# Kernel tuning notes

Measured on AMD Instinct MI355X. Metric: run time of the kernel, lower is better.

The kernel has to match this reference:

```python
import jax, jax.numpy as jnp
import numpy as np

L, H, NH, NKV, HD, S, P, FF = 2, 2048, 16, 2, 128, 1024, 1024, 5632
G = NH // NKV
THETA = 1000000.0
EPS = 1e-6
SCALE = 1.0 / np.sqrt(HD).astype(np.float32)


def rms_norm(x, w):
    return x * jax.lax.rsqrt(jnp.mean(x * x, axis=-1, keepdims=True) + EPS) * w


def rotate_half(x):
    x1, x2 = jnp.split(x, 2, axis=-1)
    return jnp.concatenate([-x2, x1], axis=-1)


def setup_inputs() -> dict:
    key = jax.random.key(0)
    ks = iter(jax.random.split(key, 16))
    w = lambda shape: jax.random.normal(next(ks), shape, jnp.float32) * 0.02
    return {
        'inputs_embeds': jax.random.normal(next(ks), (1, S, H), jnp.float32),
        'position_ids': (jnp.arange(S, dtype=jnp.int32) + P)[None, :],
        'past_k': jax.random.normal(next(ks), (L, 1, NKV, P, HD), jnp.float32),
        'past_v': jax.random.normal(next(ks), (L, 1, NKV, P, HD), jnp.float32),
        'ln1_w': jnp.ones((L, H), jnp.float32),
        'wq': w((L, H, NH * HD)), 'bq': jnp.zeros((L, NH * HD), jnp.float32),
        'wk': w((L, H, NKV * HD)), 'bk': jnp.zeros((L, NKV * HD), jnp.float32),
        'wv': w((L, H, NKV * HD)), 'bv': jnp.zeros((L, NKV * HD), jnp.float32),
        'wo': w((L, NH * HD, H)),
        'ln2_w': jnp.ones((L, H), jnp.float32),
        'w_gate': w((L, H, FF)), 'w_up': w((L, H, FF)), 'w_down': w((L, FF, H)),
        'norm_w': jnp.ones((H,), jnp.float32),
    }


def reference(inputs_embeds, position_ids, past_k, past_v, ln1_w, wq, bq, wk, bk,
              wv, bv, wo, ln2_w, w_gate, w_up, w_down, norm_w):
    pos = position_ids.astype(jnp.float32)                      # [1,S]
    inv_freq = 1.0 / (THETA ** (jnp.arange(0, HD, 2, dtype=jnp.float32) / HD))
    freqs = pos[:, :, None] * inv_freq                          # [1,S,HD/2]
    emb = jnp.concatenate([freqs, freqs], axis=-1)              # [1,S,HD]
    cos = jnp.cos(emb)[:, None]                                 # [1,1,S,HD]
    sin = jnp.sin(emb)[:, None]
    T = P + S
    k_pos = jnp.arange(T, dtype=jnp.float32)
    # causal mask over absolute positions: future keys masked with -65504
    mask = jnp.where(k_pos[None, None, None, :] > pos[:, None, :, None],
                     jnp.float32(-65504.0), jnp.float32(0.0))   # [1,1,S,T]

    hidden = inputs_embeds
    present = []
    for i in range(L):
        residual = hidden
        h = rms_norm(hidden, ln1_w[i])
        q = (h @ wq[i] + bq[i]).reshape(1, S, NH, HD).transpose(0, 2, 1, 3)
        k = (h @ wk[i] + bk[i]).reshape(1, S, NKV, HD).transpose(0, 2, 1, 3)
        v = (h @ wv[i] + bv[i]).reshape(1, S, NKV, HD).transpose(0, 2, 1, 3)
        q = q * cos + rotate_half(q) * sin
        k = k * cos + rotate_half(k) * sin
        k = jnp.concatenate([past_k[i], k], axis=2)             # [1,NKV,T,HD]
        v = jnp.concatenate([past_v[i], v], axis=2)
        present.append(k)
        present.append(v)
        # GQA: group query heads per kv head instead of expanding k/v
        qg = q.reshape(1, NKV, G, S, HD)
        attn = jnp.einsum('bkgsd,bktd->bkgst', qg, k) * SCALE   # [1,NKV,G,S,T]
        attn = jax.nn.softmax(attn + mask[:, :, None], axis=-1)
        out = jnp.einsum('bkgst,bktd->bkgsd', attn, v)
        out = out.reshape(1, NH, S, HD).transpose(0, 2, 1, 3).reshape(1, S, H)
        hidden = residual + out @ wo[i]
        residual = hidden
        h = rms_norm(hidden, ln2_w[i])
        h = (jax.nn.silu(h @ w_gate[i]) * (h @ w_up[i])) @ w_down[i]
        hidden = residual + h
    hidden = rms_norm(hidden, norm_w)
    return (hidden, *present)
```

## Files before the change

kernel.cpp:

```cpp
#include <hip/hip_runtime.h>

#define L_ 2
#define H_ 2048
#define NH_ 16
#define NKV_ 2
#define HD_ 128
#define S_ 1024
#define P_ 1024
#define T_ 2048
#define FF_ 5632
#define QKVN_ 2560
#define KOFF_ 2048
#define VOFF_ 2304

#define EPS_ 1e-6f
#define SCALE_ 0.08838834764831845f
#define DEFER_THR_ 8.0f

typedef __bf16 bf16_t;
typedef unsigned int u32;
typedef __bf16 bx8 __attribute__((ext_vector_type(8)));
typedef __bf16 bx4 __attribute__((ext_vector_type(4)));
typedef float  fx4 __attribute__((ext_vector_type(4)));

__device__ __forceinline__ fx4 mfma16(bx8 a, bx8 b, fx4 c) {
  return __builtin_amdgcn_mfma_f32_16x16x32_bf16(a, b, c, 0, 0, 0);
}

#define GLL16(gsrc, ldst) __builtin_amdgcn_global_load_lds( \
    (__attribute__((address_space(1))) void*)(gsrc),        \
    (__attribute__((address_space(3))) void*)(ldst), 16, 0, 0)

__device__ __forceinline__ bx8 lds_read_b128(char* p) {
  u32 a = (u32)(uintptr_t)(__attribute__((address_space(3))) void*)p;
  bx8 d;
  asm volatile("ds_read_b128 %0, %1" : "=v"(d) : "v"(a));
  return d;
}
__device__ __forceinline__ void lds_write_b16(char* p, float v) {
  u32 a = (u32)(uintptr_t)(__attribute__((address_space(3))) void*)p;
  bf16_t b = (bf16_t)v;
  u32 d = (u32)__builtin_bit_cast(unsigned short, b);
  asm volatile("ds_write_b16 %0, %1" :: "v"(a), "v"(d));
}

__device__ __forceinline__ int xcd_swizzle(int orig, int nwg) {
  int q = nwg >> 3, r = nwg & 7;
  int xcd = orig & 7, lid = orig >> 3;
  return (xcd < r ? xcd * (q + 1) : r * (q + 1) + (xcd - r) * q) + lid;
}

__global__ void k_rope_tables(const int* __restrict__ pos, float* __restrict__ ct, float* __restrict__ st) {
  int i = blockIdx.x * 256 + threadIdx.x;
  if (i >= S_ * 64) return;
  int s = i >> 6, d = i & 63;
  float p = (float)pos[s];
  float inv = expf(-(float)(2 * d) * (13.815510557964274f / 128.0f));
  float f = p * inv;
  ct[i] = cosf(f);
  st[i] = sinf(f);
}

__global__ void k_copy4(const float* __restrict__ in, float* __restrict__ out, int n4) {
  int i = blockIdx.x * 256 + threadIdx.x;
  if (i < n4) ((fx4*)out)[i] = ((const fx4*)in)[i];
}

__global__ void k_cbias(const float* __restrict__ bq, const float* __restrict__ bk,
                        const float* __restrict__ bv, float* __restrict__ cb) {
  int i = blockIdx.x * 256 + threadIdx.x;
  if (i >= L_ * QKVN_) return;
  int l = i / QKVN_, j = i % QKVN_;
  float v;
  if (j < KOFF_)      v = bq[l * KOFF_ + j];
  else if (j < VOFF_) v = bk[l * (NKV_ * HD_) + j - KOFF_];
  else                v = bv[l * (NKV_ * HD_) + j - VOFF_];
  cb[i] = v;
}

template<int OUTBF>
__global__ __launch_bounds__(256) void k_rmsnorm(const float* __restrict__ x, const float* __restrict__ w,
                                                 void* __restrict__ y) {
  int row = blockIdx.x, tid = threadIdx.x;
  const fx4* xr = (const fx4*)(x + (size_t)row * H_);
  fx4 v0 = xr[tid], v1 = xr[tid + 256];
  float ss = v0[0]*v0[0] + v0[1]*v0[1] + v0[2]*v0[2] + v0[3]*v0[3]
           + v1[0]*v1[0] + v1[1]*v1[1] + v1[2]*v1[2] + v1[3]*v1[3];
  #pragma unroll
  for (int off = 32; off > 0; off >>= 1) ss += __shfl_xor(ss, off);
  __shared__ float red[4];
  if ((tid & 63) == 0) red[tid >> 6] = ss;
  __syncthreads();
  float tot = red[0] + red[1] + red[2] + red[3];
  float rs = rsqrtf(tot * (1.0f / H_) + EPS_);
  const fx4* wr_ = (const fx4*)w;
  fx4 w0 = wr_[tid], w1 = wr_[tid + 256];
  if (OUTBF) {
    bf16_t* yb = (bf16_t*)y + (size_t)row * H_;
    bx4 o0, o1;
    #pragma unroll
    for (int i = 0; i < 4; i++) { o0[i] = (bf16_t)(v0[i] * rs * w0[i]); o1[i] = (bf16_t)(v1[i] * rs * w1[i]); }
    *(bx4*)&yb[tid * 4] = o0;
    *(bx4*)&yb[(tid + 256) * 4] = o1;
  } else {
    float* yf = (float*)y + (size_t)row * H_;
    fx4 o0, o1;
    #pragma unroll
    for (int i = 0; i < 4; i++) { o0[i] = v0[i] * rs * w0[i]; o1[i] = v1[i] * rs * w1[i]; }
    *(fx4*)&yf[tid * 4] = o0;
    *(fx4*)&yf[(tid + 256) * 4] = o1;
  }
}

__global__ __launch_bounds__(256) void k_transpose_w(const float* __restrict__ in, bf16_t* __restrict__ out,
                                                     int R, int C) {
  __shared__ __attribute__((aligned(16))) float Tt[64 * 68];
  int tid = threadIdx.x;
  int c0 = blockIdx.x * 64, r0 = blockIdx.y * 64;
  #pragma unroll
  for (int j = 0; j < 4; j++) {
    int c = j * 256 + tid;
    int row = c >> 4, col = (c & 15) * 4;
    *(fx4*)&Tt[row * 68 + col] = *(const fx4*)&in[(size_t)(r0 + row) * C + c0 + col];
  }
  __syncthreads();
  #pragma unroll
  for (int j = 0; j < 2; j++) {
    int c = j * 256 + tid;
    int n = c >> 3, ko = (c & 7) * 8;
    bx8 o;
    #pragma unroll
    for (int i = 0; i < 8; i++) o[i] = (bf16_t)Tt[(ko + i) * 68 + n];
    *(bx8*)&out[(size_t)(c0 + n) * R + r0 + ko] = o;
  }
}

template<int OUTBF, int HASB, int HASR>
__global__ __launch_bounds__(256) void k_gemm(const bf16_t* __restrict__ A, const bf16_t* __restrict__ Bt,
                                              const float* __restrict__ bias, const float* __restrict__ res,
                                              void* __restrict__ out, int M, int N, int K, int gy) {
  __shared__ __attribute__((aligned(16))) bf16_t sA[3][64 * 64];
  __shared__ __attribute__((aligned(16))) bf16_t sB[3][128 * 64];
  int tid = threadIdx.x;
  int w = tid >> 6, lane = tid & 63, g = lane >> 4, r = lane & 15;
  int wr = w >> 1, wc = w & 1;
  int swzid = xcd_swizzle((int)blockIdx.x, (int)gridDim.x);
  int m0 = (swzid % gy) * 64;
  int n0 = (swzid / gy) * 128;
  fx4 acc[2][4] = {};
  int swz = (r & 7) << 4;
  int col0 = (g * 16) ^ swz;
  int col1 = (64 + g * 16) ^ swz;
  int wbase = (tid & ~63) * 16;
  int nk = K >> 6;

  auto STAGE = [&](int buf, int k0) {
    #pragma unroll
    for (int j = 0; j < 2; j++) {
      int d = (j * 256 + tid) * 16;
      int row = d >> 7;
      int inrow = (d & 127) ^ ((row & 7) << 4);
      GLL16((const char*)(A + (size_t)(m0 + row) * K + k0) + inrow,
            (char*)&sA[buf][0] + j * 4096 + wbase);
    }
    #pragma unroll
    for (int j = 0; j < 4; j++) {
      int d = (j * 256 + tid) * 16;
      int row = d >> 7;
      int inrow = (d & 127) ^ ((row & 7) << 4);
      GLL16((const char*)(Bt + (size_t)(n0 + row) * K + k0) + inrow,
            (char*)&sB[buf][0] + j * 4096 + wbase);
    }
  };

  STAGE(0, 0);
  STAGE(1, 64);
  asm volatile("s_waitcnt vmcnt(6)" ::: "memory");
  __builtin_amdgcn_s_barrier();
  __builtin_amdgcn_sched_barrier(0);
  int cur = 0;
  for (int t = 0; t < nk; t++) {
    if (t + 2 < nk) STAGE((cur + 2) % 3, (t + 2) << 6);
    char* pa = (char*)&sA[cur][0] + (wr * 32 + r) * 128;
    char* pb = (char*)&sB[cur][0] + (wc * 64 + r) * 128;
    bx8 fa[2][2], fb[4][2];
    #pragma unroll
    for (int m = 0; m < 2; m++) {
      fa[m][0] = lds_read_b128(pa + m * 2048 + col0);
      fa[m][1] = lds_read_b128(pa + m * 2048 + col1);
    }
    #pragma unroll
    for (int n = 0; n < 4; n++) {
      fb[n][0] = lds_read_b128(pb + n * 2048 + col0);
      fb[n][1] = lds_read_b128(pb + n * 2048 + col1);
    }
    asm volatile("s_waitcnt lgkmcnt(0)" ::: "memory");
    __builtin_amdgcn_sched_barrier(0);
    #pragma unroll
    for (int kk = 0; kk < 2; kk++)
      #pragma unroll
      for (int n = 0; n < 4; n++) {
        acc[0][n] = mfma16(fa[0][kk], fb[n][kk], acc[0][n]);
        acc[1][n] = mfma16(fa[1][kk], fb[n][kk], acc[1][n]);
      }
    if (t + 1 < nk) {
      if (t + 2 < nk) { asm volatile("s_waitcnt vmcnt(6)" ::: "memory"); }
      else            { asm volatile("s_waitcnt vmcnt(0)" ::: "memory"); }
      __builtin_amdgcn_s_barrier();
      __builtin_amdgcn_sched_barrier(0);
    }
    cur = (cur + 1) % 3;
  }
  #pragma unroll
  for (int m = 0; m < 2; m++)
    #pragma unroll
    for (int n = 0; n < 4; n++) {
      int col = n0 + wc * 64 + n * 16 + r;
      #pragma unroll
      for (int rr = 0; rr < 4; rr++) {
        int row = m0 + wr * 32 + m * 16 + 4 * g + rr;
        float v = acc[m][n][rr];
        if (HASB) v += bias[col];
        if (HASR) v += res[(size_t)row * N + col];
        if (OUTBF) ((bf16_t*)out)[(size_t)row * N + col] = (bf16_t)v;
        else       ((float*)out)[(size_t)row * N + col] = v;
      }
    }
}

__global__ void k_rope_q(const bf16_t* __restrict__ qkv, const float* __restrict__ ct,
                         const float* __restrict__ st, bf16_t* __restrict__ qout) {
  int i = blockIdx.x * 256 + threadIdx.x;
  if (i >= S_ * NH_ * 64) return;
  int d = i & 63, h = (i >> 6) & 15, s = i >> 10;
  size_t ib = (size_t)s * QKVN_ + h * HD_;
  float x1 = (float)qkv[ib + d];
  float x2 = (float)qkv[ib + d + 64];
  float c = ct[s * 64 + d], sn = st[s * 64 + d];
  size_t ob = ((size_t)h * S_ + s) * HD_;
  qout[ob + d]      = (bf16_t)(x1 * c - x2 * sn);
  qout[ob + d + 64] = (bf16_t)(x2 * c + x1 * sn);
}

__global__ void k_build_k(const bf16_t* __restrict__ qkv, const float* __restrict__ pastk,
                          const float* __restrict__ ct, const float* __restrict__ st,
                          bf16_t* __restrict__ kc, float* __restrict__ pk_out) {
  int i = blockIdx.x * 256 + threadIdx.x;
  if (i >= NKV_ * T_ * 64) return;
  int d = i & 63, t = (i >> 6) & (T_ - 1), kv = i >> 17;
  size_t cb = ((size_t)kv * T_ + t) * HD_;
  if (t < P_) {
    size_t pb = ((size_t)kv * P_ + t) * HD_;
    float a = pastk[pb + d], b = pastk[pb + d + 64];
    kc[cb + d] = (bf16_t)a; kc[cb + d + 64] = (bf16_t)b;
    pk_out[cb + d] = a;     pk_out[cb + d + 64] = b;
  } else {
    int s = t - P_;
    size_t ib = (size_t)s * QKVN_ + KOFF_ + kv * HD_;
    float x1 = (float)qkv[ib + d];
    float x2 = (float)qkv[ib + d + 64];
    float c = ct[s * 64 + d], sn = st[s * 64 + d];
    float k1 = x1 * c - x2 * sn, k2 = x2 * c + x1 * sn;
    kc[cb + d] = (bf16_t)k1; kc[cb + d + 64] = (bf16_t)k2;
    pk_out[cb + d] = k1;     pk_out[cb + d + 64] = k2;
  }
}

__global__ __launch_bounds__(256) void k_build_vt(const bf16_t* __restrict__ qkv, const float* __restrict__ pastv,
                                                  bf16_t* __restrict__ vt, float* __restrict__ pv_out) {
  int t0 = blockIdx.x * 64, d0 = blockIdx.y * 64, kv = blockIdx.z;
  __shared__ __attribute__((aligned(16))) float Tt[64 * 68];
  int tid = threadIdx.x;
  if (t0 < P_) {
    #pragma unroll
    for (int j = 0; j < 4; j++) {
      int c = j * 256 + tid;
      int row = c >> 4, col = (c & 15) * 4;
      int t = t0 + row;
      fx4 v = *(const fx4*)&pastv[((size_t)kv * P_ + t) * HD_ + d0 + col];
      *(fx4*)&Tt[row * 68 + col] = v;
      *(fx4*)&pv_out[((size_t)kv * T_ + t) * HD_ + d0 + col] = v;
    }
  } else {
    #pragma unroll
    for (int j = 0; j < 4; j++) {
      int c = j * 256 + tid;
      int row = c >> 4, col = (c & 15) * 4;
      int t = t0 + row;
      bx4 b = *(const bx4*)&qkv[(size_t)(t - P_) * QKVN_ + VOFF_ + kv * HD_ + d0 + col];
      fx4 v;
      #pragma unroll
      for (int q = 0; q < 4; q++) v[q] = (float)b[q];
      *(fx4*)&Tt[row * 68 + col] = v;
      *(fx4*)&pv_out[((size_t)kv * T_ + t) * HD_ + d0 + col] = v;
    }
  }
  __syncthreads();
  #pragma unroll
  for (int j = 0; j < 2; j++) {
    int c = j * 256 + tid;
    int n = c >> 3, ko = (c & 7) * 8;
    bx8 o;
    #pragma unroll
    for (int i = 0; i < 8; i++) o[i] = (bf16_t)Tt[(ko + i) * 68 + n];
    *(bx8*)&vt[((size_t)kv * HD_ + d0 + n) * T_ + t0 + ko] = o;
  }
}

__global__ __launch_bounds__(256) void k_attn(const bf16_t* __restrict__ Q, const bf16_t* __restrict__ Kc,
                                              const bf16_t* __restrict__ VT, bf16_t* __restrict__ O) {
  __shared__ __attribute__((aligned(16))) bf16_t Klds[2][64 * 128];
  __shared__ __attribute__((aligned(16))) bf16_t Vlds[2][128 * 64];
  __shared__ __attribute__((aligned(16))) bf16_t Plds[4][16][72];
  int tid = threadIdx.x;
  int w = tid >> 6, lane = tid & 63, g = lane >> 4, r = lane & 15;
  int h = blockIdx.y, kv = h >> 3;
  int m0 = blockIdx.x * 64;
  int qr0 = m0 + w * 16;
  const bf16_t* qb = Q + ((size_t)h * S_ + qr0 + r) * HD_ + g * 8;
  bx8 qf[4];
  #pragma unroll
  for (int kc = 0; kc < 4; kc++) qf[kc] = *(const bx8*)(qb + kc * 32);
  fx4 of[8] = {};
  float mrun[4], lrun[4];
  #pragma unroll
  for (int i = 0; i < 4; i++) { mrun[i] = -1e30f; lrun[i] = 0.0f; }
  int lim = P_ + qr0 + 4 * g;
  int ntile = (P_ + m0 + 64) >> 6;
  const char* kg = (const char*)(Kc + (size_t)kv * T_ * HD_);
  const char* vg = (const char*)(VT + (size_t)kv * HD_ * T_);
  int wbase = (tid & ~63) * 16;

  auto STAGE = [&](int buf, int t0) {
    #pragma unroll
    for (int j = 0; j < 4; j++) {
      int D = j * 4096 + tid * 16;
      int row = D >> 8, inrow = D & 255;
      const char* src = kg + (size_t)(t0 + row) * 256 + (inrow ^ ((row & 7) << 4));
      GLL16(src, (char*)&Klds[buf][0] + j * 4096 + wbase);
    }
    #pragma unroll
    for (int j = 0; j < 4; j++) {
      int D = j * 4096 + tid * 16;
      int row = D >> 7, inrow = D & 127;
      const char* src = vg + (size_t)row * 4096 + (size_t)t0 * 2 + (inrow ^ ((row & 7) << 4));
      GLL16(src, (char*)&Vlds[buf][0] + j * 4096 + wbase);
    }
  };

  STAGE(0, 0);
  asm volatile("s_waitcnt vmcnt(0)" ::: "memory");
  __builtin_amdgcn_s_barrier();
  __builtin_amdgcn_sched_barrier(0);
  int cur = 0;
  for (int t = 0; t < ntile; t++) {
    int t0 = t * 64;
    int pref = (t + 1 < ntile);
    if (pref) {
      STAGE(cur ^ 1, t0 + 64);
      asm volatile("s_waitcnt vmcnt(8)" ::: "memory");
    } else {
      asm volatile("s_waitcnt vmcnt(0)" ::: "memory");
    }
    __builtin_amdgcn_s_barrier();
    __builtin_amdgcn_sched_barrier(0);
    char* kb = (char*)&Klds[cur][0];
    bx8 kf[4][4];
    #pragma unroll
    for (int nt = 0; nt < 4; nt++) {
      int row = nt * 16 + r;
      char* kr = kb + row * 256;
      int sz = (row & 7) << 4;
      #pragma unroll
      for (int kc = 0; kc < 4; kc++)
        kf[nt][kc] = lds_read_b128(kr + (((kc * 32 + g * 8) * 2) ^ sz));
    }
    asm volatile("s_waitcnt lgkmcnt(0)" ::: "memory");
    __builtin_amdgcn_sched_barrier(0);
    fx4 sc[4] = {};
    #pragma unroll
    for (int nt = 0; nt < 4; nt++)
      #pragma unroll
      for (int kc = 0; kc < 4; kc++)
        sc[nt] = mfma16(qf[kc], kf[nt][kc], sc[nt]);
    float lm[4] = {-1e30f, -1e30f, -1e30f, -1e30f};
    #pragma unroll
    for (int nt = 0; nt < 4; nt++)
      #pragma unroll
      for (int rr = 0; rr < 4; rr++) {
        int key = t0 + nt * 16 + r;
        float sv = sc[nt][rr] * SCALE_;
        sv = (key > lim + rr) ? -1e30f : sv;
        sc[nt][rr] = sv;
        lm[rr] = fmaxf(lm[rr], sv);
      }
    int ok = (lm[0] <= mrun[0] + DEFER_THR_) & (lm[1] <= mrun[1] + DEFER_THR_) &
             (lm[2] <= mrun[2] + DEFER_THR_) & (lm[3] <= mrun[3] + DEFER_THR_);
    if (!__all(ok)) {
      float av[4];
      #pragma unroll
      for (int off = 1; off < 16; off <<= 1)
        #pragma unroll
        for (int rr = 0; rr < 4; rr++) lm[rr] = fmaxf(lm[rr], __shfl_xor(lm[rr], off));
      #pragma unroll
      for (int rr = 0; rr < 4; rr++) {
        float mn = fmaxf(mrun[rr], lm[rr]);
        av[rr] = __expf(mrun[rr] - mn);
        mrun[rr] = mn;
        lrun[rr] *= av[rr];
      }
      #pragma unroll
      for (int f = 0; f < 8; f++)
        #pragma unroll
        for (int rr = 0; rr < 4; rr++) of[f][rr] *= av[rr];
    }
    #pragma unroll
    for (int nt = 0; nt < 4; nt++)
      #pragma unroll
      for (int rr = 0; rr < 4; rr++) {
        float pr = __expf(sc[nt][rr] - mrun[rr]);
        lrun[rr] += pr;
        lds_write_b16((char*)&Plds[w][4 * g + rr][nt * 16 + r], pr);
      }
    asm volatile("s_waitcnt lgkmcnt(0)" ::: "memory");
    __builtin_amdgcn_sched_barrier(0);
    char* vb = (char*)&Vlds[cur][0];
    #pragma unroll
    for (int ks = 0; ks < 2; ks++) {
      bx8 pa = lds_read_b128((char*)&Plds[w][r][ks * 32 + g * 8]);
      bx8 vf[8];
      #pragma unroll
      for (int dt = 0; dt < 8; dt++) {
        int row = dt * 16 + r;
        vf[dt] = lds_read_b128(vb + row * 128 + (((ks * 32 + g * 8) * 2) ^ ((row & 7) << 4)));
      }
      asm volatile("s_waitcnt lgkmcnt(0)" ::: "memory");
      __builtin_amdgcn_sched_barrier(0);
      #pragma unroll
      for (int dt = 0; dt < 8; dt++)
        of[dt] = mfma16(pa, vf[dt], of[dt]);
    }
    __builtin_amdgcn_s_barrier();
    cur ^= 1;
  }
  #pragma unroll
  for (int off = 1; off < 16; off <<= 1)
    #pragma unroll
    for (int rr = 0; rr < 4; rr++) lrun[rr] += __shfl_xor(lrun[rr], off);
  float li[4];
  #pragma unroll
  for (int rr = 0; rr < 4; rr++) li[rr] = 1.0f / lrun[rr];
  #pragma unroll
  for (int dt = 0; dt < 8; dt++)
    #pragma unroll
    for (int rr = 0; rr < 4; rr++)
      O[(size_t)(qr0 + 4 * g + rr) * H_ + h * HD_ + dt * 16 + r] = (bf16_t)(of[dt][rr] * li[rr]);
}

__global__ void k_silu_mul(const bf16_t* __restrict__ gb, const bf16_t* __restrict__ ub,
                           bf16_t* __restrict__ ob, int n8) {
  int i = blockIdx.x * 256 + threadIdx.x;
  if (i >= n8) return;
  bx8 gv = ((const bx8*)gb)[i], uv = ((const bx8*)ub)[i];
  bx8 ov;
  #pragma unroll
  for (int j = 0; j < 8; j++) {
    float x = (float)gv[j], y = (float)uv[j];
    float s = x / (1.0f + __expf(-x));
    ov[j] = (bf16_t)(s * y);
  }
  ((bx8*)ob)[i] = ov;
}

extern "C" void kernel_launch(void* const* d_in, const int* in_sizes, int n_in,
                              void* d_out, int out_size, void* d_ws, size_t ws_size,
                              hipStream_t stream) {
  const float* embeds = (const float*)d_in[0];
  const int*   pos    = (const int*)d_in[1];
  const float* past_k = (const float*)d_in[2];
  const float* past_v = (const float*)d_in[3];
  const float* ln1    = (const float*)d_in[4];
  const float* wq     = (const float*)d_in[5];
  const float* bq     = (const float*)d_in[6];
  const float* wk     = (const float*)d_in[7];
  const float* bk     = (const float*)d_in[8];
  const float* wv     = (const float*)d_in[9];
  const float* bv     = (const float*)d_in[10];
  const float* wo     = (const float*)d_in[11];
  const float* ln2    = (const float*)d_in[12];
  const float* wg     = (const float*)d_in[13];
  const float* wu     = (const float*)d_in[14];
  const float* wd     = (const float*)d_in[15];
  const float* normw  = (const float*)d_in[16];

  char* wsp = (char*)d_ws;
  auto take = [&](size_t n) { char* p = wsp; wsp += (n + 255) & ~(size_t)255; return (void*)p; };
  float*  cos_t  = (float*)take((size_t)S_ * 64 * 4);
  float*  sin_t  = (float*)take((size_t)S_ * 64 * 4);
  float*  cbias  = (float*)take((size_t)L_ * QKVN_ * 4);
  float*  hidden = (float*)take((size_t)S_ * H_ * 4);
  bf16_t* hnorm  = (bf16_t*)take((size_t)S_ * H_ * 2);
  bf16_t* qkv    = (bf16_t*)take((size_t)S_ * QKVN_ * 2);
  bf16_t* qrope  = (bf16_t*)take((size_t)NH_ * S_ * HD_ * 2);
  bf16_t* kcache = (bf16_t*)take((size_t)NKV_ * T_ * HD_ * 2);
  bf16_t* vtr    = (bf16_t*)take((size_t)NKV_ * HD_ * T_ * 2);
  bf16_t* attno  = (bf16_t*)take((size_t)S_ * H_ * 2);
  bf16_t* gateb  = (bf16_t*)take((size_t)S_ * FF_ * 2);
  bf16_t* upb    = (bf16_t*)take((size_t)S_ * FF_ * 2);
  bf16_t* hgb    = (bf16_t*)take((size_t)S_ * FF_ * 2);
  bf16_t* wT     = (bf16_t*)take((size_t)FF_ * H_ * 2);

  float* out_h = (float*)d_out;

  k_rope_tables<<<256, 256, 0, stream>>>(pos, cos_t, sin_t);
  k_cbias<<<(L_ * QKVN_ + 255) / 256, 256, 0, stream>>>(bq, bk, bv, cbias);
  k_copy4<<<(S_ * H_ / 4 + 255) / 256, 256, 0, stream>>>(embeds, hidden, S_ * H_ / 4);

  for (int l = 0; l < L_; l++) {
    const float* wq_l = wq + (size_t)l * H_ * (NH_ * HD_);
    const float* wk_l = wk + (size_t)l * H_ * (NKV_ * HD_);
    const float* wv_l = wv + (size_t)l * H_ * (NKV_ * HD_);
    const float* wo_l = wo + (size_t)l * (NH_ * HD_) * H_;
    const float* wg_l = wg + (size_t)l * H_ * FF_;
    const float* wu_l = wu + (size_t)l * H_ * FF_;
    const float* wd_l = wd + (size_t)l * FF_ * H_;
    const float* pk_in = past_k + (size_t)l * NKV_ * P_ * HD_;
    const float* pv_in = past_v + (size_t)l * NKV_ * P_ * HD_;
    float* pk_out = out_h + (size_t)S_ * H_ + (size_t)l * 2 * NKV_ * T_ * HD_;
    float* pv_out = pk_out + (size_t)NKV_ * T_ * HD_;

    k_rmsnorm<1><<<S_, 256, 0, stream>>>(hidden, ln1 + (size_t)l * H_, hnorm);
    k_transpose_w<<<dim3(32, 32), 256, 0, stream>>>(wq_l, wT, H_, NH_ * HD_);
    k_transpose_w<<<dim3(4, 32), 256, 0, stream>>>(wk_l, wT + (size_t)KOFF_ * H_, H_, NKV_ * HD_);
    k_transpose_w<<<dim3(4, 32), 256, 0, stream>>>(wv_l, wT + (size_t)VOFF_ * H_, H_, NKV_ * HD_);
    k_gemm<1, 1, 0><<<(QKVN_ / 128) * (S_ / 64), 256, 0, stream>>>(
        hnorm, wT, cbias + (size_t)l * QKVN_, nullptr, qkv, S_, QKVN_, H_, S_ / 64);
    k_rope_q<<<(S_ * NH_ * 64) / 256, 256, 0, stream>>>(qkv, cos_t, sin_t, qrope);
    k_build_k<<<(NKV_ * T_ * 64) / 256, 256, 0, stream>>>(qkv, pk_in, cos_t, sin_t, kcache, pk_out);
    k_build_vt<<<dim3(T_ / 64, HD_ / 64, NKV_), 256, 0, stream>>>(qkv, pv_in, vtr, pv_out);
    k_attn<<<dim3(S_ / 64, NH_), 256, 0, stream>>>(qrope, kcache, vtr, attno);
    k_transpose_w<<<dim3(32, 32), 256, 0, stream>>>(wo_l, wT, NH_ * HD_, H_);
    k_gemm<0, 0, 1><<<(H_ / 128) * (S_ / 64), 256, 0, stream>>>(
        attno, wT, nullptr, hidden, hidden, S_, H_, NH_ * HD_, S_ / 64);
    k_rmsnorm<1><<<S_, 256, 0, stream>>>(hidden, ln2 + (size_t)l * H_, hnorm);
    k_transpose_w<<<dim3(88, 32), 256, 0, stream>>>(wg_l, wT, H_, FF_);
    k_gemm<1, 0, 0><<<(FF_ / 128) * (S_ / 64), 256, 0, stream>>>(
        hnorm, wT, nullptr, nullptr, gateb, S_, FF_, H_, S_ / 64);
    k_transpose_w<<<dim3(88, 32), 256, 0, stream>>>(wu_l, wT, H_, FF_);
    k_gemm<1, 0, 0><<<(FF_ / 128) * (S_ / 64), 256, 0, stream>>>(
        hnorm, wT, nullptr, nullptr, upb, S_, FF_, H_, S_ / 64);
    k_silu_mul<<<(S_ * FF_ / 8) / 256, 256, 0, stream>>>(gateb, upb, hgb, S_ * FF_ / 8);
    k_transpose_w<<<dim3(32, 88), 256, 0, stream>>>(wd_l, wT, FF_, H_);
    k_gemm<0, 0, 1><<<(H_ / 128) * (S_ / 64), 256, 0, stream>>>(
        hgb, wT, nullptr, hidden, hidden, S_, H_, FF_, S_ / 64);
  }
  k_rmsnorm<0><<<S_, 256, 0, stream>>>(hidden, normw, out_h);
}
```

Measured before the change: 588.3 us.

## Fuse SiLU-mul into up GEMM epilogue and shrink attention blocks to two waves

```diff
diff --git a/kernel.cpp b/kernel.cpp
--- a/kernel.cpp
+++ b/kernel.cpp
@@ -44,6 +44,8 @@
   asm volatile("ds_write_b16 %0, %1" :: "v"(a), "v"(d));
 }
 
+#define LGKM(n) asm volatile("s_waitcnt lgkmcnt(" #n ")" ::: "memory"); __builtin_amdgcn_sched_barrier(0)
+
 __device__ __forceinline__ int xcd_swizzle(int orig, int nwg) {
   int q = nwg >> 3, r = nwg & 7;
   int xcd = orig & 7, lid = orig >> 3;
@@ -135,9 +137,10 @@
   }
 }
 
-template<int OUTBF, int HASB, int HASR>
+template<int OUTBF, int HASB, int HASR, int HASG>
 __global__ __launch_bounds__(256) void k_gemm(const bf16_t* __restrict__ A, const bf16_t* __restrict__ Bt,
                                               const float* __restrict__ bias, const float* __restrict__ res,
+                                              const bf16_t* __restrict__ gmul,
                                               void* __restrict__ out, int M, int N, int K, int gy) {
   __shared__ __attribute__((aligned(16))) bf16_t sA[3][64 * 64];
   __shared__ __attribute__((aligned(16))) bf16_t sB[3][128 * 64];
@@ -194,8 +197,7 @@
       fb[n][0] = lds_read_b128(pb + n * 2048 + col0);
       fb[n][1] = lds_read_b128(pb + n * 2048 + col1);
     }
-    asm volatile("s_waitcnt lgkmcnt(0)" ::: "memory");
-    __builtin_amdgcn_sched_barrier(0);
+    LGKM(0);
     #pragma unroll
     for (int kk = 0; kk < 2; kk++)
       #pragma unroll
@@ -222,6 +224,10 @@
         float v = acc[m][n][rr];
         if (HASB) v += bias[col];
         if (HASR) v += res[(size_t)row * N + col];
+        if (HASG) {
+          float x = (float)gmul[(size_t)row * N + col];
+          v = (x / (1.0f + __expf(-x))) * v;
+        }
         if (OUTBF) ((bf16_t*)out)[(size_t)row * N + col] = (bf16_t)v;
         else       ((float*)out)[(size_t)row * N + col] = v;
       }
@@ -307,15 +313,15 @@
   }
 }
 
-__global__ __launch_bounds__(256) void k_attn(const bf16_t* __restrict__ Q, const bf16_t* __restrict__ Kc,
+__global__ __launch_bounds__(128) void k_attn(const bf16_t* __restrict__ Q, const bf16_t* __restrict__ Kc,
                                               const bf16_t* __restrict__ VT, bf16_t* __restrict__ O) {
   __shared__ __attribute__((aligned(16))) bf16_t Klds[2][64 * 128];
   __shared__ __attribute__((aligned(16))) bf16_t Vlds[2][128 * 64];
-  __shared__ __attribute__((aligned(16))) bf16_t Plds[4][16][72];
+  __shared__ __attribute__((aligned(16))) bf16_t Plds[2][16][72];
   int tid = threadIdx.x;
   int w = tid >> 6, lane = tid & 63, g = lane >> 4, r = lane & 15;
   int h = blockIdx.y, kv = h >> 3;
-  int m0 = blockIdx.x * 64;
+  int m0 = blockIdx.x * 32;
   int qr0 = m0 + w * 16;
   const bf16_t* qb = Q + ((size_t)h * S_ + qr0 + r) * HD_ + g * 8;
   bx8 qf[4];
@@ -326,25 +332,25 @@
   #pragma unroll
   for (int i = 0; i < 4; i++) { mrun[i] = -1e30f; lrun[i] = 0.0f; }
   int lim = P_ + qr0 + 4 * g;
-  int ntile = (P_ + m0 + 64) >> 6;
+  int ntile = (P_ + m0 + 32 + 63) >> 6;
   const char* kg = (const char*)(Kc + (size_t)kv * T_ * HD_);
   const char* vg = (const char*)(VT + (size_t)kv * HD_ * T_);
   int wbase = (tid & ~63) * 16;
 
   auto STAGE = [&](int buf, int t0) {
     #pragma unroll
-    for (int j = 0; j < 4; j++) {
-      int D = j * 4096 + tid * 16;
+    for (int j = 0; j < 8; j++) {
+      int D = j * 2048 + tid * 16;
       int row = D >> 8, inrow = D & 255;
       const char* src = kg + (size_t)(t0 + row) * 256 + (inrow ^ ((row & 7) << 4));
-      GLL16(src, (char*)&Klds[buf][0] + j * 4096 + wbase);
-    }
-    #pragma unroll
-    for (int j = 0; j < 4; j++) {
-      int D = j * 4096 + tid * 16;
+      GLL16(src, (char*)&Klds[buf][0] + j * 2048 + wbase);
+    }
+    #pragma unroll
+    for (int j = 0; j < 8; j++) {
+      int D = j * 2048 + tid * 16;
       int row = D >> 7, inrow = D & 127;
       const char* src = vg + (size_t)row * 4096 + (size_t)t0 * 2 + (inrow ^ ((row & 7) << 4));
-      GLL16(src, (char*)&Vlds[buf][0] + j * 4096 + wbase);
+      GLL16(src, (char*)&Vlds[buf][0] + j * 2048 + wbase);
     }
   };
 
@@ -355,10 +361,9 @@
   int cur = 0;
   for (int t = 0; t < ntile; t++) {
     int t0 = t * 64;
-    int pref = (t + 1 < ntile);
-    if (pref) {
+    if (t + 1 < ntile) {
       STAGE(cur ^ 1, t0 + 64);
-      asm volatile("s_waitcnt vmcnt(8)" ::: "memory");
+      asm volatile("s_waitcnt vmcnt(16)" ::: "memory");
     } else {
       asm volatile("s_waitcnt vmcnt(0)" ::: "memory");
     }
@@ -375,14 +380,19 @@
       for (int kc = 0; kc < 4; kc++)
         kf[nt][kc] = lds_read_b128(kr + (((kc * 32 + g * 8) * 2) ^ sz));
     }
-    asm volatile("s_waitcnt lgkmcnt(0)" ::: "memory");
-    __builtin_amdgcn_sched_barrier(0);
     fx4 sc[4] = {};
-    #pragma unroll
-    for (int nt = 0; nt < 4; nt++)
-      #pragma unroll
-      for (int kc = 0; kc < 4; kc++)
-        sc[nt] = mfma16(qf[kc], kf[nt][kc], sc[nt]);
+    LGKM(12);
+    #pragma unroll
+    for (int kc = 0; kc < 4; kc++) sc[0] = mfma16(qf[kc], kf[0][kc], sc[0]);
+    LGKM(8);
+    #pragma unroll
+    for (int kc = 0; kc < 4; kc++) sc[1] = mfma16(qf[kc], kf[1][kc], sc[1]);
+    LGKM(4);
+    #pragma unroll
+    for (int kc = 0; kc < 4; kc++) sc[2] = mfma16(qf[kc], kf[2][kc], sc[2]);
+    LGKM(0);
+    #pragma unroll
+    for (int kc = 0; kc < 4; kc++) sc[3] = mfma16(qf[kc], kf[3][kc], sc[3]);
     float lm[4] = {-1e30f, -1e30f, -1e30f, -1e30f};
     #pragma unroll
     for (int nt = 0; nt < 4; nt++)
@@ -422,24 +432,27 @@
         lrun[rr] += pr;
         lds_write_b16((char*)&Plds[w][4 * g + rr][nt * 16 + r], pr);
       }
-    asm volatile("s_waitcnt lgkmcnt(0)" ::: "memory");
-    __builtin_amdgcn_sched_barrier(0);
+    LGKM(0);
     char* vb = (char*)&Vlds[cur][0];
-    #pragma unroll
-    for (int ks = 0; ks < 2; ks++) {
-      bx8 pa = lds_read_b128((char*)&Plds[w][r][ks * 32 + g * 8]);
-      bx8 vf[8];
-      #pragma unroll
-      for (int dt = 0; dt < 8; dt++) {
-        int row = dt * 16 + r;
-        vf[dt] = lds_read_b128(vb + row * 128 + (((ks * 32 + g * 8) * 2) ^ ((row & 7) << 4)));
-      }
-      asm volatile("s_waitcnt lgkmcnt(0)" ::: "memory");
-      __builtin_amdgcn_sched_barrier(0);
-      #pragma unroll
-      for (int dt = 0; dt < 8; dt++)
-        of[dt] = mfma16(pa, vf[dt], of[dt]);
-    }
+    bx8 pa0 = lds_read_b128((char*)&Plds[w][r][g * 8]);
+    bx8 vf0[8], vf1[8];
+    #pragma unroll
+    for (int dt = 0; dt < 8; dt++) {
+      int row = dt * 16 + r;
+      vf0[dt] = lds_read_b128(vb + row * 128 + (((g * 8) * 2) ^ ((row & 7) << 4)));
+    }
+    bx8 pa1 = lds_read_b128((char*)&Plds[w][r][32 + g * 8]);
+    #pragma unroll
+    for (int dt = 0; dt < 8; dt++) {
+      int row = dt * 16 + r;
+      vf1[dt] = lds_read_b128(vb + row * 128 + (((32 + g * 8) * 2) ^ ((row & 7) << 4)));
+    }
+    LGKM(9);
+    #pragma unroll
+    for (int dt = 0; dt < 8; dt++) of[dt] = mfma16(pa0, vf0[dt], of[dt]);
+    LGKM(0);
+    #pragma unroll
+    for (int dt = 0; dt < 8; dt++) of[dt] = mfma16(pa1, vf1[dt], of[dt]);
     __builtin_amdgcn_s_barrier();
     cur ^= 1;
   }
@@ -455,21 +468,6 @@
     #pragma unroll
     for (int rr = 0; rr < 4; rr++)
       O[(size_t)(qr0 + 4 * g + rr) * H_ + h * HD_ + dt * 16 + r] = (bf16_t)(of[dt][rr] * li[rr]);
-}
-
-__global__ void k_silu_mul(const bf16_t* __restrict__ gb, const bf16_t* __restrict__ ub,
-                           bf16_t* __restrict__ ob, int n8) {
-  int i = blockIdx.x * 256 + threadIdx.x;
-  if (i >= n8) return;
-  bx8 gv = ((const bx8*)gb)[i], uv = ((const bx8*)ub)[i];
-  bx8 ov;
-  #pragma unroll
-  for (int j = 0; j < 8; j++) {
-    float x = (float)gv[j], y = (float)uv[j];
-    float s = x / (1.0f + __expf(-x));
-    ov[j] = (bf16_t)(s * y);
-  }
-  ((bx8*)ob)[i] = ov;
 }
 
 extern "C" void kernel_launch(void* const* d_in, const int* in_sizes, int n_in,
@@ -506,7 +504,6 @@
   bf16_t* vtr    = (bf16_t*)take((size_t)NKV_ * HD_ * T_ * 2);
   bf16_t* attno  = (bf16_t*)take((size_t)S_ * H_ * 2);
   bf16_t* gateb  = (bf16_t*)take((size_t)S_ * FF_ * 2);
-  bf16_t* upb    = (bf16_t*)take((size_t)S_ * FF_ * 2);
   bf16_t* hgb    = (bf16_t*)take((size_t)S_ * FF_ * 2);
   bf16_t* wT     = (bf16_t*)take((size_t)FF_ * H_ * 2);
 
@@ -533,26 +530,25 @@
     k_transpose_w<<<dim3(32, 32), 256, 0, stream>>>(wq_l, wT, H_, NH_ * HD_);
     k_transpose_w<<<dim3(4, 32), 256, 0, stream>>>(wk_l, wT + (size_t)KOFF_ * H_, H_, NKV_ * HD_);
     k_transpose_w<<<dim3(4, 32), 256, 0, stream>>>(wv_l, wT + (size_t)VOFF_ * H_, H_, NKV_ * HD_);
-    k_gemm<1, 1, 0><<<(QKVN_ / 128) * (S_ / 64), 256, 0, stream>>>(
-        hnorm, wT, cbias + (size_t)l * QKVN_, nullptr, qkv, S_, QKVN_, H_, S_ / 64);
+    k_gemm<1, 1, 0, 0><<<(QKVN_ / 128) * (S_ / 64), 256, 0, stream>>>(
+        hnorm, wT, cbias + (size_t)l * QKVN_, nullptr, nullptr, qkv, S_, QKVN_, H_, S_ / 64);
     k_rope_q<<<(S_ * NH_ * 64) / 256, 256, 0, stream>>>(qkv, cos_t, sin_t, qrope);
     k_build_k<<<(NKV_ * T_ * 64) / 256, 256, 0, stream>>>(qkv, pk_in, cos_t, sin_t, kcache, pk_out);
     k_build_vt<<<dim3(T_ / 64, HD_ / 64, NKV_), 256, 0, stream>>>(qkv, pv_in, vtr, pv_out);
-    k_attn<<<dim3(S_ / 64, NH_), 256, 0, stream>>>(qrope, kcache, vtr, attno);
+    k_attn<<<dim3(S_ / 32, NH_), 128, 0, stream>>>(qrope, kcache, vtr, attno);
     k_transpose_w<<<dim3(32, 32), 256, 0, stream>>>(wo_l, wT, NH_ * HD_, H_);
-    k_gemm<0, 0, 1><<<(H_ / 128) * (S_ / 64), 256, 0, stream>>>(
-        attno, wT, nullptr, hidden, hidden, S_, H_, NH_ * HD_, S_ / 64);
+    k_gemm<0, 0, 1, 0><<<(H_ / 128) * (S_ / 64), 256, 0, stream>>>(
+        attno, wT, nullptr, hidden, nullptr, hidden, S_, H_, NH_ * HD_, S_ / 64);
     k_rmsnorm<1><<<S_, 256, 0, stream>>>(hidden, ln2 + (size_t)l * H_, hnorm);
     k_transpose_w<<<dim3(88, 32), 256, 0, stream>>>(wg_l, wT, H_, FF_);
-    k_gemm<1, 0, 0><<<(FF_ / 128) * (S_ / 64), 256, 0, stream>>>(
-        hnorm, wT, nullptr, nullptr, gateb, S_, FF_, H_, S_ / 64);
+    k_gemm<1, 0, 0, 0><<<(FF_ / 128) * (S_ / 64), 256, 0, stream>>>(
+        hnorm, wT, nullptr, nullptr, nullptr, gateb, S_, FF_, H_, S_ / 64);
     k_transpose_w<<<dim3(88, 32), 256, 0, stream>>>(wu_l, wT, H_, FF_);
-    k_gemm<1, 0, 0><<<(FF_ / 128) * (S_ / 64), 256, 0, stream>>>(
-        hnorm, wT, nullptr, nullptr, upb, S_, FF_, H_, S_ / 64);
-    k_silu_mul<<<(S_ * FF_ / 8) / 256, 256, 0, stream>>>(gateb, upb, hgb, S_ * FF_ / 8);
+    k_gemm<1, 0, 0, 1><<<(FF_ / 128) * (S_ / 64), 256, 0, stream>>>(
+        hnorm, wT, nullptr, nullptr, gateb, hgb, S_, FF_, H_, S_ / 64);
     k_transpose_w<<<dim3(32, 88), 256, 0, stream>>>(wd_l, wT, FF_, H_);
-    k_gemm<0, 0, 1><<<(H_ / 128) * (S_ / 64), 256, 0, stream>>>(
-        hgb, wT, nullptr, hidden, hidden, S_, H_, FF_, S_ / 64);
+    k_gemm<0, 0, 1, 0><<<(H_ / 128) * (S_ / 64), 256, 0, stream>>>(
+        hgb, wT, nullptr, hidden, nullptr, hidden, S_, H_, FF_, S_ / 64);
   }
   k_rmsnorm<0><<<S_, 256, 0, stream>>>(hidden, normw, out_h);
 }
```

After: 586.0 us. About the same (-0.4%).
